# Optimization experiments

Measured on AMD Instinct MI355X. Metric: run time of the kernel, lower is better.

## Reference

```python
import jax, jax.numpy as jnp
import numpy as np

N_NODES = 50000
N_EDGES = 800000
IN_DIM = 96
HID = 96


def setup_inputs() -> dict:
    key = jax.random.key(0)
    k1, k2, k3, k4 = jax.random.split(key, 4)
    x = jax.random.normal(k1, (N_NODES, IN_DIM), dtype=jnp.float32)
    edge_index = jax.random.randint(k2, (2, N_EDGES), 0, N_NODES, dtype=jnp.int64)
    s1 = 1.0 / np.sqrt(IN_DIM)
    s2 = 1.0 / np.sqrt(HID)
    W1 = jax.random.normal(k3, (IN_DIM, HID), dtype=jnp.float32) * s1
    b1 = jnp.zeros((HID,), dtype=jnp.float32)
    W2 = jax.random.normal(k4, (HID, HID), dtype=jnp.float32) * s2
    b2 = jnp.zeros((HID,), dtype=jnp.float32)
    return {"x": x, "edge_index": edge_index, "W1": W1, "b1": b1, "W2": W2, "b2": b2}


def _gcn_conv(x, src, dst, norm, W, b, n_nodes):
    # x' = D^{-1/2}(A+I)D^{-1/2} X W + b  (PyG GCNConv semantics)
    xw = x @ W                           # [N, out]
    msg = xw[src] * norm[:, None]        # gather + edge-normalize, [E+N, out]
    agg = jax.ops.segment_sum(msg, dst, num_segments=n_nodes)  # scatter-add
    return agg + b


def reference(x, edge_index, W1, b1, W2, b2):
    n_nodes = x.shape[0]
    loops = jnp.arange(n_nodes, dtype=edge_index.dtype)
    src = jnp.concatenate([edge_index[0], loops])  # sources (j)
    dst = jnp.concatenate([edge_index[1], loops])  # targets (i), aggregation index
    # symmetric normalization with self-loops; degree counted at targets
    deg = jax.ops.segment_sum(jnp.ones(dst.shape, dtype=x.dtype), dst, num_segments=n_nodes)
    dinv = jnp.where(deg > 0, jax.lax.rsqrt(deg), 0.0)
    norm = dinv[src] * dinv[dst]
    h = jax.nn.relu(_gcn_conv(x, src, dst, norm, W1, b1, n_nodes))
    h = jax.nn.relu(_gcn_conv(h, src, dst, norm, W2, b2, n_nodes))
    return h
```

## Files before the change

kernel.cpp:

```cpp
#include <hip/hip_runtime.h>

#define N_NODES 50000
#define N_EDGES 800000
#define DIM 96
#define FEAT_ELEMS (N_NODES * DIM)
#define NBLK 196

__device__ __forceinline__ float bf16_to_f32(unsigned short u) {
    unsigned int w = ((unsigned int)u) << 16;
    float f;
    __builtin_memcpy(&f, &w, 4);
    return f;
}
__device__ __forceinline__ unsigned short f32_to_bf16_rne(float f) {
    unsigned int w;
    __builtin_memcpy(&w, &f, 4);
    unsigned int r = (w + 0x7FFFu + ((w >> 16) & 1u)) >> 16;
    return (unsigned short)r;
}

__device__ __forceinline__ int edge_at(const void* ep, int is64, int idx) {
    if (is64) return (int)((const long long*)ep)[idx];
    return ((const int*)ep)[idx];
}

__global__ __launch_bounds__(256) void prolog_kernel(const unsigned int* edges,
                                                     const unsigned int* x,
                                                     int* flagE, int* flagF, int* cnt) {
    __shared__ unsigned int sh[256];
    int t = threadIdx.x;
    int b = blockIdx.x;
    if (b < NBLK) {
        int i = b * 256 + t;
        if (i < N_NODES) cnt[i] = 0;
        return;
    }
    if (b == NBLK) {
        if (t < 64) {
            unsigned int acc = 0;
            for (int k = 0; k < 4; ++k) {
                int idx = t * 4 + k;
                int pos = 1 + 2 * idx * 3109;
                acc |= edges[pos];
            }
            sh[t] = acc;
        }
        __syncthreads();
        if (t == 0) {
            unsigned int a = 0;
            for (int i = 0; i < 64; ++i) a |= sh[i];
            *flagE = (a == 0u) ? 1 : 0;
        }
        return;
    }
    unsigned int w = x[t * 9000];
    unsigned int e = (w >> 7) & 0xFFu;
    sh[t] = (e >= 100u && e <= 135u) ? 1u : 0u;
    __syncthreads();
    if (t == 0) {
        int c = 0;
        for (int i = 0; i < 256; ++i) c += (int)sh[i];
        *flagF = (c >= 128) ? 1 : 0;
    }
}

__global__ __launch_bounds__(256) void count_compact_kernel(const void* edges,
                                                            const int* flagE, int* cnt,
                                                            unsigned short* srcu,
                                                            unsigned short* dstu,
                                                            int* rank) {
    int e = blockIdx.x * 256 + threadIdx.x;
    if (e >= N_EDGES) return;
    int is64 = *flagE;
    int s = edge_at(edges, is64, e);
    int d = edge_at(edges, is64, N_EDGES + e);
    srcu[e] = (unsigned short)s;
    dstu[e] = (unsigned short)d;
    rank[e] = atomicAdd(&cnt[d], 1);
}

__global__ __launch_bounds__(256) void scan_blocksum_kernel(const int* cnt, int* blockSums) {
    __shared__ int sh[256];
    int i = blockIdx.x * 256 + threadIdx.x;
    sh[threadIdx.x] = (i < N_NODES) ? cnt[i] : 0;
    __syncthreads();
    for (int off = 128; off > 0; off >>= 1) {
        if (threadIdx.x < off) sh[threadIdx.x] += sh[threadIdx.x + off];
        __syncthreads();
    }
    if (threadIdx.x == 0) blockSums[blockIdx.x] = sh[0];
}

__global__ __launch_bounds__(256) void scan_offsets_kernel(const int* blockSums,
                                                           int* blockOffs, int* row_ptr) {
    __shared__ int sh[256];
    int t = threadIdx.x;
    int v = (t < NBLK) ? blockSums[t] : 0;
    sh[t] = v;
    __syncthreads();
    for (int off = 1; off < 256; off <<= 1) {
        int u = (t >= off) ? sh[t - off] : 0;
        __syncthreads();
        sh[t] += u;
        __syncthreads();
    }
    if (t < NBLK) blockOffs[t] = sh[t] - v;
    if (t == 255) row_ptr[N_NODES] = sh[255];
}

__global__ __launch_bounds__(256) void scan_apply_kernel(const int* cnt, const int* blockOffs,
                                                         int* row_ptr, float* dinv) {
    __shared__ int sh[256];
    int t = threadIdx.x;
    int i = blockIdx.x * 256 + t;
    int c = (i < N_NODES) ? cnt[i] : 0;
    sh[t] = c;
    __syncthreads();
    for (int off = 1; off < 256; off <<= 1) {
        int u = (t >= off) ? sh[t - off] : 0;
        __syncthreads();
        sh[t] += u;
        __syncthreads();
    }
    if (i < N_NODES) {
        int excl = sh[t] - c + blockOffs[blockIdx.x];
        row_ptr[i] = excl;
        dinv[i]    = rsqrtf((float)(c + 1));
    }
}

__global__ __launch_bounds__(256) void fill_direct_kernel(const unsigned short* __restrict__ dstu,
                                                          const unsigned short* __restrict__ srcu,
                                                          const int* __restrict__ rank,
                                                          const int* __restrict__ row_ptr,
                                                          unsigned short* __restrict__ csr_src) {
    int e = blockIdx.x * 256 + threadIdx.x;
    if (e >= N_EDGES) return;
    int d = dstu[e];
    int pos = row_ptr[d] + rank[e];
    csr_src[pos] = srcu[e];
}

__global__ __launch_bounds__(256) void convert_kernel(const void* x, const int* flagF,
                                                      unsigned short* xb) {
    int i4 = (blockIdx.x * 256 + threadIdx.x) * 4;
    if (i4 >= FEAT_ELEMS) return;
    int isbf16 = *flagF;
    ushort4 o;
    if (isbf16) {
        o = *(const ushort4*)((const unsigned short*)x + i4);
    } else {
        float4 v = *(const float4*)((const float*)x + i4);
        o.x = f32_to_bf16_rne(v.x);
        o.y = f32_to_bf16_rne(v.y);
        o.z = f32_to_bf16_rne(v.z);
        o.w = f32_to_bf16_rne(v.w);
    }
    *(ushort4*)(xb + i4) = o;
}

__global__ __launch_bounds__(256) void gather_kernel(const unsigned short* __restrict__ feat,
                                                     const int* __restrict__ row_ptr,
                                                     const unsigned short* __restrict__ csr_src,
                                                     const float* __restrict__ dinv,
                                                     float* __restrict__ agg) {
    int gid = blockIdx.x * 256 + threadIdx.x;
    int g = gid >> 4;
    int lane = gid & 15;
    if (g >= N_NODES) return;
    float di = dinv[g];
    int gb = g * DIM + lane * 2;
    ushort2 sv0 = *(const ushort2*)&feat[gb];
    ushort2 sv1 = *(const ushort2*)&feat[gb + 32];
    ushort2 sv2 = *(const ushort2*)&feat[gb + 64];
    float wself = di * di;
    float a0 = wself * bf16_to_f32(sv0.x), a1 = wself * bf16_to_f32(sv0.y);
    float a2 = wself * bf16_to_f32(sv1.x), a3 = wself * bf16_to_f32(sv1.y);
    float a4 = wself * bf16_to_f32(sv2.x), a5 = wself * bf16_to_f32(sv2.y);
    int e = row_ptr[g], e1 = row_ptr[g + 1];
    for (; e + 2 <= e1; e += 2) {
        int s0 = csr_src[e];
        int s1 = csr_src[e + 1];
        float w0 = dinv[s0] * di;
        float w1 = dinv[s1] * di;
        int b0 = s0 * DIM + lane * 2;
        int b1 = s1 * DIM + lane * 2;
        ushort2 p0 = *(const ushort2*)&feat[b0];
        ushort2 p1 = *(const ushort2*)&feat[b0 + 32];
        ushort2 p2 = *(const ushort2*)&feat[b0 + 64];
        ushort2 q0 = *(const ushort2*)&feat[b1];
        ushort2 q1 = *(const ushort2*)&feat[b1 + 32];
        ushort2 q2 = *(const ushort2*)&feat[b1 + 64];
        a0 = fmaf(w0, bf16_to_f32(p0.x), a0);  a1 = fmaf(w0, bf16_to_f32(p0.y), a1);
        a2 = fmaf(w0, bf16_to_f32(p1.x), a2);  a3 = fmaf(w0, bf16_to_f32(p1.y), a3);
        a4 = fmaf(w0, bf16_to_f32(p2.x), a4);  a5 = fmaf(w0, bf16_to_f32(p2.y), a5);
        a0 = fmaf(w1, bf16_to_f32(q0.x), a0);  a1 = fmaf(w1, bf16_to_f32(q0.y), a1);
        a2 = fmaf(w1, bf16_to_f32(q1.x), a2);  a3 = fmaf(w1, bf16_to_f32(q1.y), a3);
        a4 = fmaf(w1, bf16_to_f32(q2.x), a4);  a5 = fmaf(w1, bf16_to_f32(q2.y), a5);
    }
    if (e < e1) {
        int s = csr_src[e];
        float w = dinv[s] * di;
        int b0 = s * DIM + lane * 2;
        ushort2 p0 = *(const ushort2*)&feat[b0];
        ushort2 p1 = *(const ushort2*)&feat[b0 + 32];
        ushort2 p2 = *(const ushort2*)&feat[b0 + 64];
        a0 = fmaf(w, bf16_to_f32(p0.x), a0);  a1 = fmaf(w, bf16_to_f32(p0.y), a1);
        a2 = fmaf(w, bf16_to_f32(p1.x), a2);  a3 = fmaf(w, bf16_to_f32(p1.y), a3);
        a4 = fmaf(w, bf16_to_f32(p2.x), a4);  a5 = fmaf(w, bf16_to_f32(p2.y), a5);
    }
    *(float2*)&agg[gb]      = make_float2(a0, a1);
    *(float2*)&agg[gb + 32] = make_float2(a2, a3);
    *(float2*)&agg[gb + 64] = make_float2(a4, a5);
}

__global__ __launch_bounds__(256) void gemm_bias_relu_kernel(const float* A,
                                                             const void* W, const void* bias,
                                                             const int* flagF,
                                                             void* out, int outMode) {
    __shared__ float Ws[DIM * DIM];
    __shared__ float bs[DIM];
    int wBf16 = *flagF;
    int outBf16 = (outMode == 2) ? wBf16 : outMode;
    if (wBf16) {
        for (int i = threadIdx.x; i < DIM * DIM; i += 256)
            Ws[i] = bf16_to_f32(((const unsigned short*)W)[i]);
        if (threadIdx.x < DIM)
            bs[threadIdx.x] = bf16_to_f32(((const unsigned short*)bias)[threadIdx.x]);
    } else {
        const float4* W4 = (const float4*)W;
        float4* Ws4w = (float4*)Ws;
        for (int i = threadIdx.x; i < DIM * DIM / 4; i += 256) Ws4w[i] = W4[i];
        if (threadIdx.x < DIM) bs[threadIdx.x] = ((const float*)bias)[threadIdx.x];
    }
    __syncthreads();

    int colg = threadIdx.x & 7;
    int rowg = threadIdx.x >> 3;
    int row0 = blockIdx.x * 64 + rowg * 2;
    int c0 = colg * 12;

    float acc0[12], acc1[12];
    #pragma unroll
    for (int j = 0; j < 12; ++j) { acc0[j] = 0.0f; acc1[j] = 0.0f; }

    bool r0ok = (row0 < N_NODES);
    bool r1ok = (row0 + 1 < N_NODES);
    const float4* A0 = (const float4*)(A + (size_t)row0 * DIM);
    const float4* A1 = (const float4*)(A + (size_t)(row0 + 1) * DIM);
    const float4* Ws4 = (const float4*)Ws;
    const float4 z4 = make_float4(0.f, 0.f, 0.f, 0.f);

    for (int kc = 0; kc < DIM / 4; ++kc) {
        float4 a0 = r0ok ? A0[kc] : z4;
        float4 a1 = r1ok ? A1[kc] : z4;
        #pragma unroll
        for (int kk = 0; kk < 4; ++kk) {
            const float4* wrow = Ws4 + ((kc * 4 + kk) * DIM + c0) / 4;
            float4 w0 = wrow[0];
            float4 w1 = wrow[1];
            float4 w2 = wrow[2];
            float av0 = (kk == 0) ? a0.x : (kk == 1) ? a0.y : (kk == 2) ? a0.z : a0.w;
            float av1 = (kk == 0) ? a1.x : (kk == 1) ? a1.y : (kk == 2) ? a1.z : a1.w;
            acc0[0] = fmaf(av0, w0.x, acc0[0]);  acc1[0] = fmaf(av1, w0.x, acc1[0]);
            acc0[1] = fmaf(av0, w0.y, acc0[1]);  acc1[1] = fmaf(av1, w0.y, acc1[1]);
            acc0[2] = fmaf(av0, w0.z, acc0[2]);  acc1[2] = fmaf(av1, w0.z, acc1[2]);
            acc0[3] = fmaf(av0, w0.w, acc0[3]);  acc1[3] = fmaf(av1, w0.w, acc1[3]);
            acc0[4] = fmaf(av0, w1.x, acc0[4]);  acc1[4] = fmaf(av1, w1.x, acc1[4]);
            acc0[5] = fmaf(av0, w1.y, acc0[5]);  acc1[5] = fmaf(av1, w1.y, acc1[5]);
            acc0[6] = fmaf(av0, w1.z, acc0[6]);  acc1[6] = fmaf(av1, w1.z, acc1[6]);
            acc0[7] = fmaf(av0, w1.w, acc0[7]);  acc1[7] = fmaf(av1, w1.w, acc1[7]);
            acc0[8] = fmaf(av0, w2.x, acc0[8]);  acc1[8] = fmaf(av1, w2.x, acc1[8]);
            acc0[9] = fmaf(av0, w2.y, acc0[9]);  acc1[9] = fmaf(av1, w2.y, acc1[9]);
            acc0[10] = fmaf(av0, w2.z, acc0[10]); acc1[10] = fmaf(av1, w2.z, acc1[10]);
            acc0[11] = fmaf(av0, w2.w, acc0[11]); acc1[11] = fmaf(av1, w2.w, acc1[11]);
        }
    }

    #pragma unroll
    for (int r = 0; r < 2; ++r) {
        int row = row0 + r;
        if (row >= N_NODES) continue;
        float* accp = (r == 0) ? acc0 : acc1;
        int ob = row * DIM + c0;
        if (outBf16) {
            #pragma unroll
            for (int j = 0; j < 12; ++j) {
                float v = fmaxf(accp[j] + bs[c0 + j], 0.0f);
                ((unsigned short*)out)[ob + j] = f32_to_bf16_rne(v);
            }
        } else {
            float4 o[3];
            #pragma unroll
            for (int q = 0; q < 3; ++q) {
                o[q].x = fmaxf(accp[q * 4 + 0] + bs[c0 + q * 4 + 0], 0.0f);
                o[q].y = fmaxf(accp[q * 4 + 1] + bs[c0 + q * 4 + 1], 0.0f);
                o[q].z = fmaxf(accp[q * 4 + 2] + bs[c0 + q * 4 + 2], 0.0f);
                o[q].w = fmaxf(accp[q * 4 + 3] + bs[c0 + q * 4 + 3], 0.0f);
            }
            float4* op = (float4*)((float*)out + ob);
            op[0] = o[0]; op[1] = o[1]; op[2] = o[2];
        }
    }
}

extern "C" void kernel_launch(void* const* d_in, const int* in_sizes, int n_in,
                              void* d_out, int out_size, void* d_ws, size_t ws_size,
                              hipStream_t stream) {
    const void* x  = d_in[0];
    const void* ei = d_in[1];
    const void* W1 = d_in[2];
    const void* b1 = d_in[3];
    const void* W2 = d_in[4];
    const void* b2 = d_in[5];

    char* base = (char*)d_ws;
    size_t off = 0;
    auto carve = [&](size_t bytes) -> void* {
        void* p = base + off;
        off += (bytes + 255) & ~(size_t)255;
        return p;
    };
    int*            flagE     = (int*)carve(4);
    int*            flagF     = (int*)carve(4);
    int*            cnt       = (int*)carve((size_t)N_NODES * 4);
    int*            row_ptr   = (int*)carve((size_t)(N_NODES + 1) * 4);
    float*          dinv      = (float*)carve((size_t)N_NODES * 4);
    int*            blockSums = (int*)carve((size_t)NBLK * 4);
    int*            blockOffs = (int*)carve((size_t)NBLK * 4);
    unsigned short* srcu      = (unsigned short*)carve((size_t)N_EDGES * 2);
    unsigned short* dstu      = (unsigned short*)carve((size_t)N_EDGES * 2);
    int*            rank      = (int*)carve((size_t)N_EDGES * 4);
    unsigned short* csr_src   = (unsigned short*)carve((size_t)N_EDGES * 2);
    float*          agg       = (float*)carve((size_t)FEAT_ELEMS * 4);
    unsigned short* xb        = (unsigned short*)carve((size_t)FEAT_ELEMS * 2);
    unsigned short* h         = (unsigned short*)carve((size_t)FEAT_ELEMS * 2);

    const int egrid = (N_EDGES + 255) / 256;
    const int cgrid = (FEAT_ELEMS / 4 + 255) / 256;
    const int agrid = (N_NODES * 16 + 255) / 256;
    const int ggrid = (N_NODES + 63) / 64;

    prolog_kernel<<<NBLK + 2, 256, 0, stream>>>((const unsigned int*)ei,
                                                (const unsigned int*)x, flagE, flagF, cnt);
    count_compact_kernel<<<egrid, 256, 0, stream>>>(ei, flagE, cnt, srcu, dstu, rank);
    scan_blocksum_kernel<<<NBLK, 256, 0, stream>>>(cnt, blockSums);
    scan_offsets_kernel<<<1, 256, 0, stream>>>(blockSums, blockOffs, row_ptr);
    scan_apply_kernel<<<NBLK, 256, 0, stream>>>(cnt, blockOffs, row_ptr, dinv);
    fill_direct_kernel<<<egrid, 256, 0, stream>>>(dstu, srcu, rank, row_ptr, csr_src);
    convert_kernel<<<cgrid, 256, 0, stream>>>(x, flagF, xb);

    gather_kernel<<<agrid, 256, 0, stream>>>(xb, row_ptr, csr_src, dinv, agg);
    gemm_bias_relu_kernel<<<ggrid, 256, 0, stream>>>(agg, W1, b1, flagF, h, 1);

    gather_kernel<<<agrid, 256, 0, stream>>>(h, row_ptr, csr_src, dinv, agg);
    gemm_bias_relu_kernel<<<ggrid, 256, 0, stream>>>(agg, W2, b2, flagF, d_out, 2);
}
```

Before: 246.8 us.

## Use bf16 MFMA for GEMM, store aggregates in bf16, shrink rank array

Replaces the scalar FP32 GEMM with a bf16 MFMA 16x16x32 kernel. Weights are converted to bf16 and swizzled in LDS into the MFMA B-fragment layout. The gather kernel now writes its aggregates as bf16 instead of fp32, which halves the intermediate traffic and feeds the MFMA directly. The per-edge rank array is narrowed to 16-bit to cut memory traffic. Together these trade some extra rounding in the aggregate and weights for less bandwidth and compute in the GEMM stages. The output stores are now scalar per element rather than vectorized.

```diff
diff --git a/kernel.cpp b/kernel.cpp
--- a/kernel.cpp
+++ b/kernel.cpp
@@ -5,6 +5,9 @@
 #define DIM 96
 #define FEAT_ELEMS (N_NODES * DIM)
 #define NBLK 196
+
+typedef __attribute__((ext_vector_type(8))) short short8;
+typedef __attribute__((ext_vector_type(4))) float float4v;
 
 __device__ __forceinline__ float bf16_to_f32(unsigned short u) {
     unsigned int w = ((unsigned int)u) << 16;
@@ -68,7 +71,7 @@
                                                             const int* flagE, int* cnt,
                                                             unsigned short* srcu,
                                                             unsigned short* dstu,
-                                                            int* rank) {
+                                                            unsigned short* rank) {
     int e = blockIdx.x * 256 + threadIdx.x;
     if (e >= N_EDGES) return;
     int is64 = *flagE;
@@ -76,7 +79,7 @@
     int d = edge_at(edges, is64, N_EDGES + e);
     srcu[e] = (unsigned short)s;
     dstu[e] = (unsigned short)d;
-    rank[e] = atomicAdd(&cnt[d], 1);
+    rank[e] = (unsigned short)atomicAdd(&cnt[d], 1);
 }
 
 __global__ __launch_bounds__(256) void scan_blocksum_kernel(const int* cnt, int* blockSums) {
@@ -131,13 +134,13 @@
 
 __global__ __launch_bounds__(256) void fill_direct_kernel(const unsigned short* __restrict__ dstu,
                                                           const unsigned short* __restrict__ srcu,
-                                                          const int* __restrict__ rank,
+                                                          const unsigned short* __restrict__ rank,
                                                           const int* __restrict__ row_ptr,
                                                           unsigned short* __restrict__ csr_src) {
     int e = blockIdx.x * 256 + threadIdx.x;
     if (e >= N_EDGES) return;
     int d = dstu[e];
-    int pos = row_ptr[d] + rank[e];
+    int pos = row_ptr[d] + (int)rank[e];
     csr_src[pos] = srcu[e];
 }
 
@@ -163,7 +166,7 @@
                                                      const int* __restrict__ row_ptr,
                                                      const unsigned short* __restrict__ csr_src,
                                                      const float* __restrict__ dinv,
-                                                     float* __restrict__ agg) {
+                                                     unsigned short* __restrict__ aggb) {
     int gid = blockIdx.x * 256 + threadIdx.x;
     int g = gid >> 4;
     int lane = gid & 15;
@@ -209,97 +212,95 @@
         a2 = fmaf(w, bf16_to_f32(p1.x), a2);  a3 = fmaf(w, bf16_to_f32(p1.y), a3);
         a4 = fmaf(w, bf16_to_f32(p2.x), a4);  a5 = fmaf(w, bf16_to_f32(p2.y), a5);
     }
-    *(float2*)&agg[gb]      = make_float2(a0, a1);
-    *(float2*)&agg[gb + 32] = make_float2(a2, a3);
-    *(float2*)&agg[gb + 64] = make_float2(a4, a5);
-}
-
-__global__ __launch_bounds__(256) void gemm_bias_relu_kernel(const float* A,
-                                                             const void* W, const void* bias,
-                                                             const int* flagF,
-                                                             void* out, int outMode) {
-    __shared__ float Ws[DIM * DIM];
+    unsigned int o0 = (unsigned int)f32_to_bf16_rne(a0) | ((unsigned int)f32_to_bf16_rne(a1) << 16);
+    unsigned int o1 = (unsigned int)f32_to_bf16_rne(a2) | ((unsigned int)f32_to_bf16_rne(a3) << 16);
+    unsigned int o2 = (unsigned int)f32_to_bf16_rne(a4) | ((unsigned int)f32_to_bf16_rne(a5) << 16);
+    *(unsigned int*)&aggb[gb]      = o0;
+    *(unsigned int*)&aggb[gb + 32] = o1;
+    *(unsigned int*)&aggb[gb + 64] = o2;
+}
+
+__global__ __launch_bounds__(256) void gemm_mfma_kernel(const unsigned short* __restrict__ A,
+                                                        const void* W, const void* bias,
+                                                        const int* flagF,
+                                                        void* out, int outMode) {
+    __shared__ unsigned short Wlin[DIM * DIM];
+    __shared__ unsigned short Wsw[3 * 6 * 64 * 8];
     __shared__ float bs[DIM];
     int wBf16 = *flagF;
     int outBf16 = (outMode == 2) ? wBf16 : outMode;
+
     if (wBf16) {
-        for (int i = threadIdx.x; i < DIM * DIM; i += 256)
-            Ws[i] = bf16_to_f32(((const unsigned short*)W)[i]);
+        const ushort4* W4 = (const ushort4*)W;
+        ushort4* L4 = (ushort4*)Wlin;
+        for (int i = threadIdx.x; i < DIM * DIM / 4; i += 256) L4[i] = W4[i];
         if (threadIdx.x < DIM)
             bs[threadIdx.x] = bf16_to_f32(((const unsigned short*)bias)[threadIdx.x]);
     } else {
-        const float4* W4 = (const float4*)W;
-        float4* Ws4w = (float4*)Ws;
-        for (int i = threadIdx.x; i < DIM * DIM / 4; i += 256) Ws4w[i] = W4[i];
+        const float* Wf = (const float*)W;
+        for (int i = threadIdx.x; i < DIM * DIM; i += 256) Wlin[i] = f32_to_bf16_rne(Wf[i]);
         if (threadIdx.x < DIM) bs[threadIdx.x] = ((const float*)bias)[threadIdx.x];
     }
     __syncthreads();
 
-    int colg = threadIdx.x & 7;
-    int rowg = threadIdx.x >> 3;
-    int row0 = blockIdx.x * 64 + rowg * 2;
-    int c0 = colg * 12;
-
-    float acc0[12], acc1[12];
+    for (int f = threadIdx.x; f < 1152; f += 256) {
+        int kt = f / 384;
+        int rem = f - kt * 384;
+        int nt = rem >> 6;
+        int ln64 = rem & 63;
+        int q = ln64 >> 4, ln = ln64 & 15;
+        int k0 = kt * 32 + q * 8;
+        int n = nt * 16 + ln;
+        unsigned int w0 = (unsigned int)Wlin[(k0 + 0) * DIM + n] |
+                          ((unsigned int)Wlin[(k0 + 1) * DIM + n] << 16);
+        unsigned int w1 = (unsigned int)Wlin[(k0 + 2) * DIM + n] |
+                          ((unsigned int)Wlin[(k0 + 3) * DIM + n] << 16);
+        unsigned int w2 = (unsigned int)Wlin[(k0 + 4) * DIM + n] |
+                          ((unsigned int)Wlin[(k0 + 5) * DIM + n] << 16);
+        unsigned int w3 = (unsigned int)Wlin[(k0 + 6) * DIM + n] |
+                          ((unsigned int)Wlin[(k0 + 7) * DIM + n] << 16);
+        uint4 pk = make_uint4(w0, w1, w2, w3);
+        *(uint4*)&Wsw[f * 8] = pk;
+    }
+    __syncthreads();
+
+    int wave = threadIdx.x >> 6;
+    int lane = threadIdx.x & 63;
+    int quad = lane >> 4, ln = lane & 15;
+    int m0 = blockIdx.x * 64 + wave * 16;
+    int arow = m0 + ln;
+    bool arowok = (arow < N_NODES);
+
+    float4v acc[6];
     #pragma unroll
-    for (int j = 0; j < 12; ++j) { acc0[j] = 0.0f; acc1[j] = 0.0f; }
-
-    bool r0ok = (row0 < N_NODES);
-    bool r1ok = (row0 + 1 < N_NODES);
-    const float4* A0 = (const float4*)(A + (size_t)row0 * DIM);
-    const float4* A1 = (const float4*)(A + (size_t)(row0 + 1) * DIM);
-    const float4* Ws4 = (const float4*)Ws;
-    const float4 z4 = make_float4(0.f, 0.f, 0.f, 0.f);
-
-    for (int kc = 0; kc < DIM / 4; ++kc) {
-        float4 a0 = r0ok ? A0[kc] : z4;
-        float4 a1 = r1ok ? A1[kc] : z4;
+    for (int nt = 0; nt < 6; ++nt) acc[nt] = (float4v){0.f, 0.f, 0.f, 0.f};
+
+    #pragma unroll
+    for (int kt = 0; kt < 3; ++kt) {
+        short8 af;
+        if (arowok) {
+            af = *(const short8*)&A[arow * DIM + kt * 32 + quad * 8];
+        } else {
+            af = (short8){0, 0, 0, 0, 0, 0, 0, 0};
+        }
         #pragma unroll
-        for (int kk = 0; kk < 4; ++kk) {
-            const float4* wrow = Ws4 + ((kc * 4 + kk) * DIM + c0) / 4;
-            float4 w0 = wrow[0];
-            float4 w1 = wrow[1];
-            float4 w2 = wrow[2];
-            float av0 = (kk == 0) ? a0.x : (kk == 1) ? a0.y : (kk == 2) ? a0.z : a0.w;
-            float av1 = (kk == 0) ? a1.x : (kk == 1) ? a1.y : (kk == 2) ? a1.z : a1.w;
-            acc0[0] = fmaf(av0, w0.x, acc0[0]);  acc1[0] = fmaf(av1, w0.x, acc1[0]);
-            acc0[1] = fmaf(av0, w0.y, acc0[1]);  acc1[1] = fmaf(av1, w0.y, acc1[1]);
-            acc0[2] = fmaf(av0, w0.z, acc0[2]);  acc1[2] = fmaf(av1, w0.z, acc1[2]);
-            acc0[3] = fmaf(av0, w0.w, acc0[3]);  acc1[3] = fmaf(av1, w0.w, acc1[3]);
-            acc0[4] = fmaf(av0, w1.x, acc0[4]);  acc1[4] = fmaf(av1, w1.x, acc1[4]);
-            acc0[5] = fmaf(av0, w1.y, acc0[5]);  acc1[5] = fmaf(av1, w1.y, acc1[5]);
-            acc0[6] = fmaf(av0, w1.z, acc0[6]);  acc1[6] = fmaf(av1, w1.z, acc1[6]);
-            acc0[7] = fmaf(av0, w1.w, acc0[7]);  acc1[7] = fmaf(av1, w1.w, acc1[7]);
-            acc0[8] = fmaf(av0, w2.x, acc0[8]);  acc1[8] = fmaf(av1, w2.x, acc1[8]);
-            acc0[9] = fmaf(av0, w2.y, acc0[9]);  acc1[9] = fmaf(av1, w2.y, acc1[9]);
-            acc0[10] = fmaf(av0, w2.z, acc0[10]); acc1[10] = fmaf(av1, w2.z, acc1[10]);
-            acc0[11] = fmaf(av0, w2.w, acc0[11]); acc1[11] = fmaf(av1, w2.w, acc1[11]);
+        for (int nt = 0; nt < 6; ++nt) {
+            short8 bf = *(const short8*)&Wsw[((kt * 6 + nt) * 64 + lane) * 8];
+            acc[nt] = __builtin_amdgcn_mfma_f32_16x16x32_bf16(af, bf, acc[nt], 0, 0, 0);
         }
     }
 
     #pragma unroll
-    for (int r = 0; r < 2; ++r) {
-        int row = row0 + r;
-        if (row >= N_NODES) continue;
-        float* accp = (r == 0) ? acc0 : acc1;
-        int ob = row * DIM + c0;
-        if (outBf16) {
-            #pragma unroll
-            for (int j = 0; j < 12; ++j) {
-                float v = fmaxf(accp[j] + bs[c0 + j], 0.0f);
-                ((unsigned short*)out)[ob + j] = f32_to_bf16_rne(v);
-            }
-        } else {
-            float4 o[3];
-            #pragma unroll
-            for (int q = 0; q < 3; ++q) {
-                o[q].x = fmaxf(accp[q * 4 + 0] + bs[c0 + q * 4 + 0], 0.0f);
-                o[q].y = fmaxf(accp[q * 4 + 1] + bs[c0 + q * 4 + 1], 0.0f);
-                o[q].z = fmaxf(accp[q * 4 + 2] + bs[c0 + q * 4 + 2], 0.0f);
-                o[q].w = fmaxf(accp[q * 4 + 3] + bs[c0 + q * 4 + 3], 0.0f);
-            }
-            float4* op = (float4*)((float*)out + ob);
-            op[0] = o[0]; op[1] = o[1]; op[2] = o[2];
+    for (int nt = 0; nt < 6; ++nt) {
+        int n = nt * 16 + ln;
+        float bv = bs[n];
+        #pragma unroll
+        for (int reg = 0; reg < 4; ++reg) {
+            int row = m0 + quad * 4 + reg;
+            if (row >= N_NODES) continue;
+            float v = fmaxf(acc[nt][reg] + bv, 0.0f);
+            if (outBf16) ((unsigned short*)out)[row * DIM + n] = f32_to_bf16_rne(v);
+            else         ((float*)out)[row * DIM + n] = v;
         }
     }
 }
@@ -330,9 +331,9 @@
     int*            blockOffs = (int*)carve((size_t)NBLK * 4);
     unsigned short* srcu      = (unsigned short*)carve((size_t)N_EDGES * 2);
     unsigned short* dstu      = (unsigned short*)carve((size_t)N_EDGES * 2);
-    int*            rank      = (int*)carve((size_t)N_EDGES * 4);
+    unsigned short* rank      = (unsigned short*)carve((size_t)N_EDGES * 2);
     unsigned short* csr_src   = (unsigned short*)carve((size_t)N_EDGES * 2);
-    float*          agg       = (float*)carve((size_t)FEAT_ELEMS * 4);
+    unsigned short* aggb      = (unsigned short*)carve((size_t)FEAT_ELEMS * 2);
     unsigned short* xb        = (unsigned short*)carve((size_t)FEAT_ELEMS * 2);
     unsigned short* h         = (unsigned short*)carve((size_t)FEAT_ELEMS * 2);
 
@@ -350,9 +351,9 @@
     fill_direct_kernel<<<egrid, 256, 0, stream>>>(dstu, srcu, rank, row_ptr, csr_src);
     convert_kernel<<<cgrid, 256, 0, stream>>>(x, flagF, xb);
 
-    gather_kernel<<<agrid, 256, 0, stream>>>(xb, row_ptr, csr_src, dinv, agg);
-    gemm_bias_relu_kernel<<<ggrid, 256, 0, stream>>>(agg, W1, b1, flagF, h, 1);
-
-    gather_kernel<<<agrid, 256, 0, stream>>>(h, row_ptr, csr_src, dinv, agg);
-    gemm_bias_relu_kernel<<<ggrid, 256, 0, stream>>>(agg, W2, b2, flagF, d_out, 2);
-}
+    gather_kernel<<<agrid, 256, 0, stream>>>(xb, row_ptr, csr_src, dinv, aggb);
+    gemm_mfma_kernel<<<ggrid, 256, 0, stream>>>(aggb, W1, b1, flagF, h, 1);
+
+    gather_kernel<<<agrid, 256, 0, stream>>>(h, row_ptr, csr_src, dinv, aggb);
+    gemm_mfma_kernel<<<ggrid, 256, 0, stream>>>(aggb, W2, b2, flagF, d_out, 2);
+}
```

After: 212.3 us. 1.16x faster.
